# Performance work log

Measured on AMD Instinct MI355X. Metric: run time of the kernel, lower is better.

The kernel has to match this reference:

```python
import jax, jax.numpy as jnp
import numpy as np

B, S, H = 2, 2048, 2048
HK, HV, DK, DV, K = 16, 32, 128, 128, 4
KEY_DIM = HK * DK          # 2048
VAL_DIM = HV * DV          # 4096
CONV_DIM = 2 * KEY_DIM + VAL_DIM  # 8192
EPS = 1e-6


def setup_inputs() -> dict:
    key = jax.random.key(0)
    ks = jax.random.split(key, 8)
    n = lambda k, sh, s=1.0: jax.random.normal(k, sh, dtype=jnp.float32) * s
    return {
        "hidden_states": n(ks[0], (B, S, H)),
        "w_qkvz": n(ks[1], (H, 2 * KEY_DIM + 2 * VAL_DIM), 0.02),
        "w_ba": n(ks[2], (H, 2 * HV), 0.02),
        "conv_w": n(ks[3], (CONV_DIM, K), 0.5),
        "A_log": jnp.log(jax.random.uniform(ks[4], (HV,), minval=1e-3, maxval=16.0)),
        "dt_bias": jnp.ones((HV,), jnp.float32),
        "norm_w": jnp.ones((DV,), jnp.float32),
        "w_out": n(ks[5], (VAL_DIM, H), 0.02),
    }


def _l2norm(x):
    return x * jax.lax.rsqrt(jnp.sum(x * x, axis=-1, keepdims=True) + EPS)


def _softplus_thr(x, threshold=20.0):
    # fused_gdn_gating: softplus with linear tail beyond threshold (beta=1)
    return jnp.where(x <= threshold, jnp.log1p(jnp.exp(jnp.minimum(x, threshold))), x)


def reference(hidden_states, w_qkvz, w_ba, conv_w, A_log, dt_bias, norm_w, w_out):
    ratio = HV // HK  # v-heads per k-head (GVA)
    # --- projections + qkvz/ba split (fix_query_key_value_ordering) ---
    qkvz = (hidden_states @ w_qkvz).reshape(B, S, HK, 2 * DK + 2 * ratio * DV)
    q = qkvz[..., :DK]                                   # [B,S,HK,DK]
    k = qkvz[..., DK:2 * DK]
    v = qkvz[..., 2 * DK:2 * DK + ratio * DV]
    z = qkvz[..., 2 * DK + ratio * DV:].reshape(B, S, HV, DV)
    ba = (hidden_states @ w_ba).reshape(B, S, HK, 2 * ratio)
    b = ba[..., :ratio].reshape(B, S, HV)
    a = ba[..., ratio:].reshape(B, S, HV)
    # --- causal depthwise conv1d over time on cat(q,k,v), then SiLU ---
    mixed = jnp.concatenate([q.reshape(B, S, KEY_DIM), k.reshape(B, S, KEY_DIM),
                             v.reshape(B, S, VAL_DIM)], axis=-1)  # [B,S,CONV_DIM]
    xp = jnp.pad(mixed, ((0, 0), (K - 1, 0), (0, 0)))
    conv = sum(xp[:, j:j + S, :] * conv_w[:, j] for j in range(K))
    conv = jax.nn.silu(conv)
    q = _l2norm(conv[..., :KEY_DIM].reshape(B, S, HK, DK))
    k = _l2norm(conv[..., KEY_DIM:2 * KEY_DIM].reshape(B, S, HK, DK))
    v = conv[..., 2 * KEY_DIM:].reshape(B, S, HV, DV)
    q = jnp.repeat(q, ratio, axis=2)  # [B,S,HV,DK]
    k = jnp.repeat(k, ratio, axis=2)
    # --- gating: g = -exp(A_log) * softplus(a + dt_bias); beta = sigmoid(b) ---
    g = -jnp.exp(A_log) * _softplus_thr(a + dt_bias)   # [B,S,HV]
    beta = jax.nn.sigmoid(b)                            # [B,S,HV]
    scale = DK ** -0.5

    # --- gated delta rule recurrence over time ---
    def step(Sst, inp):
        qt, kt, vt, gt, bt = inp            # [B,HV,*]
        Sst = Sst * jnp.exp(gt)[..., None, None]
        kv = jnp.einsum('bhk,bhkv->bhv', kt, Sst)
        Sst = Sst + jnp.einsum('bhk,bhv->bhkv', kt, bt[..., None] * (vt - kv))
        o = jnp.einsum('bhk,bhkv->bhv', qt * scale, Sst)
        return Sst, o

    xs = (q.transpose(1, 0, 2, 3), k.transpose(1, 0, 2, 3), v.transpose(1, 0, 2, 3),
          g.transpose(1, 0, 2), beta.transpose(1, 0, 2))
    S0 = jnp.zeros((B, HV, DK, DV), jnp.float32)
    _, o = jax.lax.scan(step, S0, xs)
    core = o.transpose(1, 0, 2, 3)  # [B,S,HV,DV]
    # --- gated RMSNorm (norm before gate): rmsnorm(x)*w * silu(z) ---
    core_n = core * jax.lax.rsqrt(jnp.mean(core * core, axis=-1, keepdims=True) + EPS)
    y = core_n * norm_w * jax.nn.silu(z)
    # --- out projection ---
    return y.reshape(B, S, VAL_DIM) @ w_out
```

## Files before the change

### kernel.cpp

```cpp
#include <hip/hip_runtime.h>

typedef unsigned short u16;
typedef unsigned int u32;

typedef __attribute__((ext_vector_type(8))) short bf16x8;
typedef __attribute__((ext_vector_type(4))) float f32x4;
typedef __attribute__((ext_vector_type(2))) float f32x2;

__device__ __forceinline__ float bf2f(u16 v) {
    union { u32 i; float f; } u; u.i = ((u32)v) << 16; return u.f;
}
__device__ __forceinline__ u16 f2bf(float f) {
    union { float f; u32 i; } u; u.f = f;
    u32 r = u.i + 0x7FFFu + ((u.i >> 16) & 1u);
    return (u16)(r >> 16);
}
__device__ __forceinline__ u32 pack2(float lo, float hi) {
    return (u32)f2bf(lo) | ((u32)f2bf(hi) << 16);
}
__device__ __forceinline__ void unpack8(uint4 r, float* o) {
    o[0] = __uint_as_float(r.x << 16); o[1] = __uint_as_float(r.x & 0xffff0000u);
    o[2] = __uint_as_float(r.y << 16); o[3] = __uint_as_float(r.y & 0xffff0000u);
    o[4] = __uint_as_float(r.z << 16); o[5] = __uint_as_float(r.z & 0xffff0000u);
    o[6] = __uint_as_float(r.w << 16); o[7] = __uint_as_float(r.w & 0xffff0000u);
}
__device__ __forceinline__ void async16(const void* g, void* l) {
    __builtin_amdgcn_global_load_lds((const __attribute__((address_space(1))) void*)g,
                                     (__attribute__((address_space(3))) void*)l, 16, 0, 0);
}
template<int CTRL>
__device__ __forceinline__ float dpp_add(float x) {
    int y = __builtin_amdgcn_update_dpp(0, __float_as_int(x), CTRL, 0xf, 0xf, true);
    return x + __int_as_float(y);
}
__device__ __forceinline__ float row16_allreduce(float x) {
    x = dpp_add<0xB1>(x);
    x = dpp_add<0x4E>(x);
    x = dpp_add<0x141>(x);
    x = dpp_add<0x140>(x);
    return x;
}

__global__ __launch_bounds__(256) void f2b_kernel(const float* __restrict__ in,
                                                  u16* __restrict__ out)
{
    long i = ((long)blockIdx.x * 256 + threadIdx.x) * 8;
    float4 a = *(const float4*)&in[i], b = *(const float4*)&in[i + 4];
    uint4 o = make_uint4(pack2(a.x, a.y), pack2(a.z, a.w), pack2(b.x, b.y), pack2(b.z, b.w));
    *(uint4*)&out[i] = o;
}

__global__ __launch_bounds__(256) void transpose_f2b(const float* __restrict__ in,
                                                     u16* __restrict__ out, int R, int C)
{
    __shared__ float tile[32][33];
    const int r0 = blockIdx.y * 32, c0 = blockIdx.x * 32;
    const int tr = threadIdx.x >> 3;
    const int tc = (threadIdx.x & 7) * 4;
    float4 v = *(const float4*)&in[(long)(r0 + tr) * C + c0 + tc];
    tile[tr][tc] = v.x; tile[tr][tc + 1] = v.y; tile[tr][tc + 2] = v.z; tile[tr][tc + 3] = v.w;
    __syncthreads();
    uint2 o;
    o.x = pack2(tile[tc][tr], tile[tc + 1][tr]);
    o.y = pack2(tile[tc + 2][tr], tile[tc + 3][tr]);
    *(uint2*)&out[(long)(c0 + tr) * R + r0 + tc] = o;
}

template<int CF>
__global__ __launch_bounds__(256) void gemm_bt(const u16* __restrict__ A,
                                               const u16* __restrict__ Bt,
                                               void* __restrict__ Cp,
                                               void* __restrict__ Cp2,
                                               int M, int N, int K)
{
    __shared__ __align__(16) u16 As[128 * 32];
    __shared__ __align__(16) u16 Bs[128 * 32];

    const int tid = threadIdx.x;
    const int lane = tid & 63;
    const int wave = tid >> 6;
    const int wm = (wave >> 1) * 64;
    const int wn = (wave & 1) * 64;
    const int lanelo = lane & 15;
    const int quad = lane >> 4;
    const long m0 = (long)blockIdx.y * 128;
    const long n0 = (long)blockIdx.x * 128;

    f32x4 acc[4][4];
#pragma unroll
    for (int i = 0; i < 4; ++i)
#pragma unroll
        for (int j = 0; j < 4; ++j) acc[i][j] = (f32x4)0.0f;

    const u16* agp0 = A + (long)(m0 + wave * 16 + (lane >> 2)) * K + (lane & 3) * 8;
    const u16* agp1 = agp0 + 64 * (long)K;
    const u16* bgp0 = Bt + (long)(n0 + wave * 16 + (lane >> 2)) * K + (lane & 3) * 8;
    const u16* bgp1 = bgp0 + 64 * (long)K;
    u16* lA0 = &As[wave * 16 * 32];
    u16* lA1 = &As[(wave * 16 + 64) * 32];
    u16* lB0 = &Bs[wave * 16 * 32];
    u16* lB1 = &Bs[(wave * 16 + 64) * 32];

    for (int k0 = 0; k0 < K; k0 += 32) {
        __syncthreads();
        async16(agp0 + k0, lA0);
        async16(agp1 + k0, lA1);
        async16(bgp0 + k0, lB0);
        async16(bgp1 + k0, lB1);
        __syncthreads();

        bf16x8 af[4], bf[4];
#pragma unroll
        for (int mt = 0; mt < 4; ++mt)
            af[mt] = *(const bf16x8*)&As[(wm + mt * 16 + lanelo) * 32 + quad * 8];
#pragma unroll
        for (int nt = 0; nt < 4; ++nt)
            bf[nt] = *(const bf16x8*)&Bs[(wn + nt * 16 + lanelo) * 32 + quad * 8];
#pragma unroll
        for (int mt = 0; mt < 4; ++mt)
#pragma unroll
            for (int nt = 0; nt < 4; ++nt)
                acc[mt][nt] = __builtin_amdgcn_mfma_f32_16x16x32_bf16(af[mt], bf[nt], acc[mt][nt], 0, 0, 0);
    }

#pragma unroll
    for (int nt = 0; nt < 4; ++nt) {
        const long col = n0 + wn + nt * 16 + lanelo;
        int hkq = 0, rr = 0;
        if constexpr (CF == 2) { hkq = (int)col / 768; rr = (int)col - hkq * 768; }
#pragma unroll
        for (int mt = 0; mt < 4; ++mt)
#pragma unroll
            for (int r = 0; r < 4; ++r) {
                long row = m0 + wm + mt * 16 + quad * 4 + r;
                if constexpr (CF == 1)      ((float*)Cp)[row * N + col] = acc[mt][nt][r];
                else if constexpr (CF == 0) ((u16*)Cp)[row * N + col] = f2bf(acc[mt][nt][r]);
                else {
                    u16 vv = f2bf(acc[mt][nt][r]);
                    if (rr < 512) ((u16*)Cp )[row * 8192 + hkq * 512 + rr] = vv;
                    else          ((u16*)Cp2)[row * 4096 + hkq * 256 + (rr - 512)] = vv;
                }
            }
    }
}

__global__ __launch_bounds__(256) void ba_kernel(const float* __restrict__ hs,
                                                 const float* __restrict__ wba,
                                                 const float* __restrict__ A_log,
                                                 const float* __restrict__ dt_bias,
                                                 float* __restrict__ gbuf,
                                                 float* __restrict__ bbuf)
{
    const int m = blockIdx.x * 4 + (threadIdx.x >> 6);
    const int n = threadIdx.x & 63;
    const float* hrow = &hs[(long)m * 2048];
    float acc = 0.f;
#pragma unroll 8
    for (int k = 0; k < 2048; ++k)
        acc += hrow[k] * wba[(long)k * 64 + n];
    const int hk4 = n >> 2, r = n & 3;
    if (r < 2) {
        bbuf[(long)m * 32 + hk4 * 2 + r] = 1.f / (1.f + expf(-acc));
    } else {
        const int hv = hk4 * 2 + (r - 2);
        float x = acc + dt_bias[hv];
        float sp = (x > 20.f) ? x : log1pf(expf(x));
        gbuf[(long)m * 32 + hv] = -expf(A_log[hv]) * sp;
    }
}

__global__ __launch_bounds__(256) void conv_kernel(const u16* __restrict__ qkvb,
                                                   const float* __restrict__ cw,
                                                   u16* __restrict__ qfb,
                                                   u16* __restrict__ kfb,
                                                   u16* __restrict__ vbuf)
{
    const int bid = blockIdx.x;
    const int bs = bid >> 2, part = bid & 3;
    const int c = part * 2048 + threadIdx.x * 8;
    int n;
    if (c < 2048)       n = (c >> 7) * 512 + (c & 127);
    else if (c < 4096) { int c2 = c - 2048; n = (c2 >> 7) * 512 + 128 + (c2 & 127); }
    else               { int c2 = c - 4096; n = (c2 >> 8) * 512 + 256 + (c2 & 255); }
    const int s = bs & 2047;
    const long base = (long)bs * 8192 + n;

    float x0[8], x1[8], x2[8], x3[8];
#pragma unroll
    for (int i = 0; i < 8; ++i) { x0[i] = 0.f; x1[i] = 0.f; x2[i] = 0.f; }
    { uint4 r = *(const uint4*)&qkvb[base]; unpack8(r, x3); }
    if (s >= 1) { uint4 r = *(const uint4*)&qkvb[base - 8192];     unpack8(r, x2); }
    if (s >= 2) { uint4 r = *(const uint4*)&qkvb[base - 2 * 8192]; unpack8(r, x1); }
    if (s >= 3) { uint4 r = *(const uint4*)&qkvb[base - 3 * 8192]; unpack8(r, x0); }

    float v[8]; float ss = 0.f;
#pragma unroll
    for (int i = 0; i < 8; ++i) {
        float4 w = *(const float4*)&cw[(c + i) * 4];
        float a = x0[i] * w.x + x1[i] * w.y + x2[i] * w.z + x3[i] * w.w;
        v[i] = a / (1.f + expf(-a));
        ss += v[i] * v[i];
    }
    if (part < 2) {
        ss = row16_allreduce(ss);
        float rn = rsqrtf(ss + 1e-6f);
#pragma unroll
        for (int i = 0; i < 8; ++i) v[i] *= rn;
        u16* dst = (part == 0 ? qfb : kfb) + (long)bs * 2048 + (c & 2047);
        uint4 o = make_uint4(pack2(v[0], v[1]), pack2(v[2], v[3]), pack2(v[4], v[5]), pack2(v[6], v[7]));
        *(uint4*)dst = o;
    } else {
        uint4 o = make_uint4(pack2(v[0], v[1]), pack2(v[2], v[3]), pack2(v[4], v[5]), pack2(v[6], v[7]));
        *(uint4*)&vbuf[(long)bs * 4096 + (c - 4096)] = o;
    }
}


#define KL_S 136
#define KT_S 40
#define TL_S 40
#define GL_S 40
#define RT_S 40
#define SBT_S 136
#define SF_S 132
#define SCALE_QK 0.08838834764831845f

__global__ __launch_bounds__(64) void prep_kernel(const u16* __restrict__ kfb,
                                                  const float* __restrict__ gbuf,
                                                  const float* __restrict__ bbuf,
                                                  u16* __restrict__ Tbuf,
                                                  float* __restrict__ Cbuf)
{
    __shared__ __align__(16) u16 Kl[32 * KL_S];
    __shared__ __align__(16) float Lf[32 * 33];
    __shared__ __align__(16) float Tt[32 * 32];
    __shared__ float garr[32], barr[32], Gc[32];

    const int bid = blockIdx.x;
    const int b = bid >> 11, h = (bid >> 6) & 31, tile = bid & 63;
    const int hk = h >> 1;
    const int tid = threadIdx.x;
    const int lanelo = tid & 15, quad = tid >> 4;
    const long rowbase = (long)b * 2048 + tile * 32;

    {
        const int row = tid >> 1, half = tid & 1;
        const u16* src = &kfb[(rowbase + row) * 2048 + hk * 128 + half * 64];
#pragma unroll
        for (int i = 0; i < 8; ++i) {
            uint4 v = *(const uint4*)(src + i * 8);
            *(uint4*)&Kl[row * KL_S + half * 64 + i * 8] = v;
        }
    }
    if (tid < 32) {
        garr[tid] = gbuf[(rowbase + tid) * 32 + h];
        barr[tid] = bbuf[(rowbase + tid) * 32 + h];
    }
    __syncthreads();
    if (tid == 0) {
        float a = 0.f;
        for (int t = 0; t < 32; ++t) { a += garr[t]; Gc[t] = a; }
    }
    __syncthreads();

    f32x4 cc[2][2];
#pragma unroll
    for (int mt = 0; mt < 2; ++mt)
#pragma unroll
        for (int nt = 0; nt < 2; ++nt) cc[mt][nt] = (f32x4)0.f;
#pragma unroll
    for (int kt = 0; kt < 4; ++kt) {
        bf16x8 a0 = *(const bf16x8*)&Kl[(0 * 16 + lanelo) * KL_S + kt * 32 + quad * 8];
        bf16x8 a1 = *(const bf16x8*)&Kl[(1 * 16 + lanelo) * KL_S + kt * 32 + quad * 8];
        cc[0][0] = __builtin_amdgcn_mfma_f32_16x16x32_bf16(a0, a0, cc[0][0], 0, 0, 0);
        cc[0][1] = __builtin_amdgcn_mfma_f32_16x16x32_bf16(a0, a1, cc[0][1], 0, 0, 0);
        cc[1][0] = __builtin_amdgcn_mfma_f32_16x16x32_bf16(a1, a0, cc[1][0], 0, 0, 0);
        cc[1][1] = __builtin_amdgcn_mfma_f32_16x16x32_bf16(a1, a1, cc[1][1], 0, 0, 0);
    }
#pragma unroll
    for (int mt = 0; mt < 2; ++mt)
#pragma unroll
        for (int nt = 0; nt < 2; ++nt)
#pragma unroll
            for (int r = 0; r < 4; ++r) {
                const int t = mt * 16 + quad * 4 + r, j = nt * 16 + lanelo;
                float L = (j < t) ? barr[t] * __expf(Gc[t] - Gc[j]) * cc[mt][nt][r] : 0.f;
                Lf[t * 33 + j] = L;
            }
    __syncthreads();

    if (tid < 32) {
        const int c = tid;
        float T[32];
#pragma unroll
        for (int t = 0; t < 32; ++t) {
            float s = (t == c) ? 1.f : 0.f;
#pragma unroll
            for (int j = 0; j < t; ++j) s -= Lf[t * 33 + j] * T[j];
            T[t] = s;
        }
#pragma unroll
        for (int t = 0; t < 32; ++t) Tt[t * 32 + c] = T[t];
    }
    if (tid < 32) {
        const float G31 = Gc[31];
        const float eg = __expf(Gc[tid]);
        float* cb = &Cbuf[(long)bid * 256];
        cb[tid]       = barr[tid];
        cb[32 + tid]  = barr[tid] * eg;
        cb[64 + tid]  = SCALE_QK * eg;
        cb[96 + tid]  = __expf(G31 - Gc[tid]);
        cb[128 + tid] = Gc[tid];
        if (tid == 0) cb[192] = __expf(G31);
    }
    __syncthreads();
    {
        const float* tp = &Tt[tid * 16];
        u32 hi[8], lo[8];
#pragma unroll
        for (int i = 0; i < 8; ++i) {
            u16 h0 = f2bf(tp[2 * i]),     h1 = f2bf(tp[2 * i + 1]);
            float l0 = tp[2 * i] - bf2f(h0), l1 = tp[2 * i + 1] - bf2f(h1);
            hi[i] = (u32)h0 | ((u32)h1 << 16);
            lo[i] = pack2(l0, l1);
        }
        u16* dst = &Tbuf[(long)bid * 2048 + tid * 16];
        *(uint4*)dst       = make_uint4(hi[0], hi[1], hi[2], hi[3]);
        *(uint4*)(dst + 8) = make_uint4(hi[4], hi[5], hi[6], hi[7]);
        u16* dstl = dst + 1024;
        *(uint4*)dstl       = make_uint4(lo[0], lo[1], lo[2], lo[3]);
        *(uint4*)(dstl + 8) = make_uint4(lo[4], lo[5], lo[6], lo[7]);
    }
}

__global__ __launch_bounds__(256) void scan_kernel(const u16* __restrict__ kfb,
                                                   const u16* __restrict__ qfb,
                                                   const u16* __restrict__ vbuf,
                                                   const u16* __restrict__ Tbuf,
                                                   const float* __restrict__ Cbuf,
                                                   u16* __restrict__ obuf)
{
    __shared__ __align__(16) u16 Kl[32 * KL_S];
    __shared__ __align__(16) u16 Ql[32 * KL_S];
    __shared__ __align__(16) u16 KTl[128 * KT_S];
    __shared__ __align__(16) u16 Tl[64 * TL_S];
    __shared__ __align__(16) u16 Gl[32 * GL_S];
    __shared__ __align__(16) u16 RTl[16 * RT_S];
    __shared__ __align__(16) u16 DTl[16 * RT_S];
    __shared__ __align__(16) u16 DTs[16 * RT_S];
    __shared__ __align__(16) u16 Sbt[16 * SBT_S];
    __shared__ __align__(16) float Sf[16 * SF_S];
    __shared__ __align__(16) u16 Vl[32 * 16];
    __shared__ __align__(16) float Cf[256];

    const int bid = blockIdx.x;
    const int b = bid >> 8;
    const int h = (bid >> 3) & 31;
    const int c0 = (bid & 7) * 16;
    const int hk = h >> 1;
    const int tid = threadIdx.x;
    const int lane = tid & 63;
    const int w = tid >> 6;
    const int lanelo = lane & 15;
    const int quad = lane >> 4;
    const long rowbase = (long)b * 2048;
    const long tIdxBase = ((long)(b * 32 + h)) * 64;

    for (int i = tid; i < 16 * SF_S; i += 256) Sf[i] = 0.f;
    for (int i = tid; i < 16 * SBT_S; i += 256) Sbt[i] = 0;
    __syncthreads();

    const int srow = tid >> 3, scp = tid & 7;
    const u16* kg = &kfb[(rowbase + srow) * 2048 + hk * 128 + scp * 16];
    const u16* qg = &qfb[(rowbase + srow) * 2048 + hk * 128 + scp * 16];
    const int mtQK = w >> 1, ntQK = w & 1;
    const int mtY = w & 1;
    const bool isY = (w < 2);

    for (int tile = 0; tile < 64; ++tile) {
        const int t0 = tile * 32;
        uint4 k0 = *(const uint4*)(kg + (long)t0 * 2048);
        uint4 k1 = *(const uint4*)(kg + (long)t0 * 2048 + 8);
        uint4 q0 = *(const uint4*)(qg + (long)t0 * 2048);
        uint4 q1 = *(const uint4*)(qg + (long)t0 * 2048 + 8);
        uint4 tt = *(const uint4*)&Tbuf[(tIdxBase + tile) * 2048 + tid * 8];
        if (w == 0) {
            const int r = tid >> 1, c8 = (tid & 1) * 8;
            async16(&vbuf[(rowbase + t0 + r) * 4096 + h * 128 + c0 + c8], &Vl[tid * 8]);
        } else if (w == 1) {
            const int u = tid - 64;
            async16(&Cbuf[(tIdxBase + tile) * 256 + u * 4], &Cf[u * 4]);
        }
        *(uint4*)&Kl[srow * KL_S + scp * 16] = k0;
        *(uint4*)&Kl[srow * KL_S + scp * 16 + 8] = k1;
        *(uint4*)&Ql[srow * KL_S + scp * 16] = q0;
        *(uint4*)&Ql[srow * KL_S + scp * 16 + 8] = q1;
        {
            u32 ws_[8] = { k0.x, k0.y, k0.z, k0.w, k1.x, k1.y, k1.z, k1.w };
#pragma unroll
            for (int i = 0; i < 8; ++i) {
                KTl[(scp * 16 + 2 * i) * KT_S + srow] = (u16)(ws_[i] & 0xffffu);
                KTl[(scp * 16 + 2 * i + 1) * KT_S + srow] = (u16)(ws_[i] >> 16);
            }
        }
        {
            const int r = tid >> 2, c8 = (tid & 3) * 8;
            *(uint4*)&Tl[r * TL_S + c8] = tt;
        }
        __syncthreads();

        f32x4 qk = (f32x4)0.f;
#pragma unroll
        for (int kt = 0; kt < 4; ++kt) {
            bf16x8 aq = *(const bf16x8*)&Ql[(mtQK * 16 + lanelo) * KL_S + kt * 32 + quad * 8];
            bf16x8 bk = *(const bf16x8*)&Kl[(ntQK * 16 + lanelo) * KL_S + kt * 32 + quad * 8];
            qk = __builtin_amdgcn_mfma_f32_16x16x32_bf16(aq, bk, qk, 0, 0, 0);
        }
        const u16* aYsrc = isY ? Kl : Ql;
        f32x4 yo = (f32x4)0.f;
#pragma unroll
        for (int kt = 0; kt < 4; ++kt) {
            bf16x8 a = *(const bf16x8*)&aYsrc[(mtY * 16 + lanelo) * KL_S + kt * 32 + quad * 8];
            bf16x8 bs = *(const bf16x8*)&Sbt[lanelo * SBT_S + kt * 32 + quad * 8];
            yo = __builtin_amdgcn_mfma_f32_16x16x32_bf16(a, bs, yo, 0, 0, 0);
        }
        {
            f32x4 gt4 = *(const f32x4*)&Cf[128 + mtQK * 16 + quad * 4];
            float gj = Cf[128 + ntQK * 16 + lanelo];
#pragma unroll
            for (int r = 0; r < 4; ++r) {
                const int t = mtQK * 16 + quad * 4 + r, j = ntQK * 16 + lanelo;
                float gv = (j <= t) ? qk[r] * __expf(gt4[r] - gj) * SCALE_QK : 0.f;
                Gl[t * GL_S + j] = f2bf(gv);
            }
        }
        if (isY) {
            f32x4 bt4 = *(const f32x4*)&Cf[0 + mtY * 16 + quad * 4];
            f32x4 bg4 = *(const f32x4*)&Cf[32 + mtY * 16 + quad * 4];
            float rv[4];
#pragma unroll
            for (int r = 0; r < 4; ++r) {
                float vv = bf2f(Vl[(mtY * 16 + quad * 4 + r) * 16 + lanelo]);
                rv[r] = bt4[r] * vv - bg4[r] * yo[r];
            }
            *(uint2*)&RTl[lanelo * RT_S + mtY * 16 + quad * 4] =
                make_uint2(pack2(rv[0], rv[1]), pack2(rv[2], rv[3]));
        }
        __syncthreads();

        if (isY) {
            bf16x8 ath = *(const bf16x8*)&Tl[(mtY * 16 + lanelo) * TL_S + quad * 8];
            bf16x8 atl = *(const bf16x8*)&Tl[(32 + mtY * 16 + lanelo) * TL_S + quad * 8];
            bf16x8 br  = *(const bf16x8*)&RTl[lanelo * RT_S + quad * 8];
            f32x4 dl = __builtin_amdgcn_mfma_f32_16x16x32_bf16(ath, br, (f32x4)0.f, 0, 0, 0);
            dl = __builtin_amdgcn_mfma_f32_16x16x32_bf16(atl, br, dl, 0, 0, 0);
            f32x4 ec4 = *(const f32x4*)&Cf[96 + mtY * 16 + quad * 4];
            *(uint2*)&DTl[lanelo * RT_S + mtY * 16 + quad * 4] =
                make_uint2(pack2(dl[0], dl[1]), pack2(dl[2], dl[3]));
            *(uint2*)&DTs[lanelo * RT_S + mtY * 16 + quad * 4] =
                make_uint2(pack2(dl[0] * ec4[0], dl[1] * ec4[1]),
                           pack2(dl[2] * ec4[2], dl[3] * ec4[3]));
        }
        __syncthreads();

        if (!isY) {
            const int mt = w - 2;
            bf16x8 ag = *(const bf16x8*)&Gl[(mt * 16 + lanelo) * GL_S + quad * 8];
            bf16x8 bd = *(const bf16x8*)&DTl[lanelo * RT_S + quad * 8];
            f32x4 oi = __builtin_amdgcn_mfma_f32_16x16x32_bf16(ag, bd, (f32x4)0.f, 0, 0, 0);
            f32x4 so4 = *(const f32x4*)&Cf[64 + mt * 16 + quad * 4];
#pragma unroll
            for (int r = 0; r < 4; ++r) {
                float ov = so4[r] * yo[r] + oi[r];
                obuf[((rowbase + t0 + mt * 16 + quad * 4 + r) * 32 + h) * 128 + c0 + lanelo] = f2bf(ov);
            }
        }
        const float gC = Cf[192];
#pragma unroll
        for (int s = 0; s < 2; ++s) {
            const int mt = w * 2 + s;
            bf16x8 ak = *(const bf16x8*)&KTl[(mt * 16 + lanelo) * KT_S + quad * 8];
            bf16x8 bd = *(const bf16x8*)&DTs[lanelo * RT_S + quad * 8];
            f32x4 ds4 = __builtin_amdgcn_mfma_f32_16x16x32_bf16(ak, bd, (f32x4)0.f, 0, 0, 0);
            float* sp = &Sf[lanelo * SF_S + mt * 16 + quad * 4];
            f32x4 sv = *(const f32x4*)sp;
#pragma unroll
            for (int r = 0; r < 4; ++r) sv[r] = gC * sv[r] + ds4[r];
            *(f32x4*)sp = sv;
            *(uint2*)&Sbt[lanelo * SBT_S + mt * 16 + quad * 4] =
                make_uint2(pack2(sv[0], sv[1]), pack2(sv[2], sv[3]));
        }
        __syncthreads();
    }
}

__global__ __launch_bounds__(128) void gate_kernel(const u16* __restrict__ obuf,
                                                   const u16* __restrict__ zbuf,
                                                   const float* __restrict__ norm_w,
                                                   u16* __restrict__ ybuf)
{
    const int bid = blockIdx.x;
    const int bs = bid >> 5, hv = bid & 31;
    const int dv = threadIdx.x;
    __shared__ float red[2];
    float v = bf2f(obuf[(long)bid * 128 + dv]);
    float ss = v * v;
    ss += __shfl_xor(ss, 1);  ss += __shfl_xor(ss, 2);  ss += __shfl_xor(ss, 4);
    ss += __shfl_xor(ss, 8);  ss += __shfl_xor(ss, 16); ss += __shfl_xor(ss, 32);
    if ((dv & 63) == 0) red[dv >> 6] = ss;
    __syncthreads();
    const float mean = (red[0] + red[1]) * (1.f / 128.f);
    const float rstd = rsqrtf(mean + 1e-6f);
    const int hk = hv >> 1;
    const float z = bf2f(zbuf[(long)bs * 4096 + hk * 256 + (hv & 1) * 128 + dv]);
    const float y = v * rstd * norm_w[dv] * (z / (1.f + expf(-z)));
    ybuf[(long)bs * 4096 + hv * 128 + dv] = f2bf(y);
}

extern "C" void kernel_launch(void* const* d_in, const int* in_sizes, int n_in,
                              void* d_out, int out_size, void* d_ws, size_t ws_size,
                              hipStream_t stream)
{
    const float* hs      = (const float*)d_in[0];
    const float* w_qkvz  = (const float*)d_in[1];
    const float* w_ba    = (const float*)d_in[2];
    const float* conv_w  = (const float*)d_in[3];
    const float* A_log   = (const float*)d_in[4];
    const float* dt_bias = (const float*)d_in[5];
    const float* norm_w  = (const float*)d_in[6];
    const float* w_out   = (const float*)d_in[7];

    char* ws = (char*)d_ws;
    u16*   qkvb  = (u16*)ws;
    u16*   kfb   = (u16*)(ws + 67108864);
    u16*   qfb   = (u16*)(ws + 83886080);
    u16*   vbuf  = (u16*)(ws + 100663296);
    u16*   Tbuf  = (u16*)(ws + 134217728);
    float* Cbuf  = (float*)(ws + 150994944);
    float* gbuf  = (float*)(ws + 155189248);
    float* bbuf  = (float*)(ws + 155713536);
    u16*   zbuf  = (u16*)(ws + 156237824);
    u16*   wqkvz_t = (u16*)(ws + 67108864);
    u16*   hs_b    = (u16*)(ws + 117440512);
    u16*   obuf    = (u16*)ws;
    u16*   wout_t  = (u16*)(ws + 33554432);
    u16*   ybuf    = (u16*)(ws + 67108864);

    f2b_kernel<<<4096, 256, 0, stream>>>(hs, hs_b);
    transpose_f2b<<<dim3(384, 64), 256, 0, stream>>>(w_qkvz, wqkvz_t, 2048, 12288);
    gemm_bt<2><<<dim3(96, 32), 256, 0, stream>>>(hs_b, wqkvz_t, qkvb, zbuf, 4096, 12288, 2048);
    ba_kernel<<<1024, 256, 0, stream>>>(hs, w_ba, A_log, dt_bias, gbuf, bbuf);
    conv_kernel<<<4096 * 4, 256, 0, stream>>>(qkvb, conv_w, qfb, kfb, vbuf);
    prep_kernel<<<4096, 64, 0, stream>>>(kfb, gbuf, bbuf, Tbuf, Cbuf);
    scan_kernel<<<512, 256, 0, stream>>>(kfb, qfb, vbuf, Tbuf, Cbuf, obuf);
    transpose_f2b<<<dim3(64, 128), 256, 0, stream>>>(w_out, wout_t, 4096, 2048);
    gate_kernel<<<4096 * 32, 128, 0, stream>>>(obuf, zbuf, norm_w, ybuf);
    gemm_bt<1><<<dim3(16, 32), 256, 0, stream>>>(ybuf, wout_t, d_out, nullptr, 4096, 2048, 4096);
}
```

Baseline: 1.033 ms.

## Add 256x256 double-buffered swizzled GEMM for the qkvz projection

Replaces the 128x128-tile GEMM for the large qkvz projection with a new kernel that uses 256x256 tiles, 512 threads, and double-buffered async LDS loads with an XOR-swizzled layout. It also adds workgroup-order swizzling for L2 locality and raises MFMA priority with s_setprio. The goal is more data reuse per tile and fewer LDS bank conflicts. In exchange it needs 128KB of LDS and heavy register use, which limits occupancy, and it launches only 768 workgroups.

```diff
diff --git a/kernel.cpp b/kernel.cpp
--- a/kernel.cpp
+++ b/kernel.cpp
@@ -126,20 +126,114 @@
 #pragma unroll
     for (int nt = 0; nt < 4; ++nt) {
         const long col = n0 + wn + nt * 16 + lanelo;
-        int hkq = 0, rr = 0;
-        if constexpr (CF == 2) { hkq = (int)col / 768; rr = (int)col - hkq * 768; }
 #pragma unroll
         for (int mt = 0; mt < 4; ++mt)
 #pragma unroll
             for (int r = 0; r < 4; ++r) {
                 long row = m0 + wm + mt * 16 + quad * 4 + r;
                 if constexpr (CF == 1)      ((float*)Cp)[row * N + col] = acc[mt][nt][r];
-                else if constexpr (CF == 0) ((u16*)Cp)[row * N + col] = f2bf(acc[mt][nt][r]);
-                else {
-                    u16 vv = f2bf(acc[mt][nt][r]);
-                    if (rr < 512) ((u16*)Cp )[row * 8192 + hkq * 512 + rr] = vv;
-                    else          ((u16*)Cp2)[row * 4096 + hkq * 256 + (rr - 512)] = vv;
-                }
+                else                        ((u16*)Cp)[row * N + col] = f2bf(acc[mt][nt][r]);
+            }
+    }
+}
+
+__global__ __launch_bounds__(512, 2) void gemm256_bt(const u16* __restrict__ A,
+                                                     const u16* __restrict__ Bt,
+                                                     void* __restrict__ Cp,
+                                                     void* __restrict__ Cp2,
+                                                     int M, int N, int K)
+{
+    __shared__ __align__(16) u16 As[2][256 * 64];
+    __shared__ __align__(16) u16 Bs[2][256 * 64];
+
+    const int tid = threadIdx.x;
+    const int lane = tid & 63;
+    const int w = tid >> 6;
+    const int wm = w >> 2;
+    const int wn = w & 3;
+    const int lanelo = lane & 15;
+    const int quad = lane >> 4;
+
+    const int nx = gridDim.x;
+    const int nwg = nx * gridDim.y;
+    const int orig = blockIdx.y * nx + blockIdx.x;
+    const int cpx = nwg >> 3;
+    const int swz = (orig & 7) * cpx + (orig >> 3);
+    const long n0 = (long)(swz % nx) * 256;
+    const long m0 = (long)(swz / nx) * 256;
+
+    f32x4 acc[8][4];
+#pragma unroll
+    for (int i = 0; i < 8; ++i)
+#pragma unroll
+        for (int j = 0; j < 4; ++j) acc[i][j] = (f32x4)0.0f;
+
+    const int kt_n = K >> 6;
+
+    auto stage = [&](int buf, int kt) {
+        const int k0 = kt << 6;
+#pragma unroll
+        for (int r = 0; r < 4; ++r) {
+            const int c = r * 512 + tid;
+            const int row = c >> 3, ci = c & 7;
+            const int gcol = ((ci ^ (row & 7)) << 3);
+            async16(&A[(m0 + row) * (long)K + k0 + gcol], &As[buf][c * 8]);
+        }
+#pragma unroll
+        for (int r = 0; r < 4; ++r) {
+            const int c = r * 512 + tid;
+            const int row = c >> 3, ci = c & 7;
+            const int gcol = ((ci ^ (row & 7)) << 3);
+            async16(&Bt[(n0 + row) * (long)K + k0 + gcol], &Bs[buf][c * 8]);
+        }
+    };
+
+    int buf = 0;
+    stage(0, 0);
+    __syncthreads();
+
+    for (int kt = 0; kt < kt_n; ++kt) {
+        if (kt + 1 < kt_n) stage(buf ^ 1, kt + 1);
+#pragma unroll
+        for (int kk = 0; kk < 2; ++kk) {
+            bf16x8 a[8], b[4];
+#pragma unroll
+            for (int mf = 0; mf < 8; ++mf) {
+                const int row = wm * 128 + mf * 16 + lanelo;
+                const int ci = (kk * 4 + quad) ^ (row & 7);
+                a[mf] = *(const bf16x8*)&As[buf][row * 64 + ci * 8];
+            }
+#pragma unroll
+            for (int nf = 0; nf < 4; ++nf) {
+                const int row = wn * 64 + nf * 16 + lanelo;
+                const int ci = (kk * 4 + quad) ^ (row & 7);
+                b[nf] = *(const bf16x8*)&Bs[buf][row * 64 + ci * 8];
+            }
+            __builtin_amdgcn_s_setprio(1);
+#pragma unroll
+            for (int mf = 0; mf < 8; ++mf)
+#pragma unroll
+                for (int nf = 0; nf < 4; ++nf)
+                    acc[mf][nf] = __builtin_amdgcn_mfma_f32_16x16x32_bf16(a[mf], b[nf], acc[mf][nf], 0, 0, 0);
+            __builtin_amdgcn_s_setprio(0);
+        }
+        __syncthreads();
+        buf ^= 1;
+    }
+
+#pragma unroll
+    for (int nf = 0; nf < 4; ++nf) {
+        const long col = n0 + wn * 64 + nf * 16 + lanelo;
+        const int hkq = (int)col / 768;
+        const int rr = (int)col - hkq * 768;
+#pragma unroll
+        for (int mf = 0; mf < 8; ++mf)
+#pragma unroll
+            for (int r = 0; r < 4; ++r) {
+                const long row = m0 + wm * 128 + mf * 16 + quad * 4 + r;
+                const u16 vv = f2bf(acc[mf][nf][r]);
+                if (rr < 512) ((u16*)Cp )[row * 8192 + hkq * 512 + rr] = vv;
+                else          ((u16*)Cp2)[row * 4096 + hkq * 256 + (rr - 512)] = vv;
             }
     }
 }
@@ -548,7 +642,7 @@
 
     f2b_kernel<<<4096, 256, 0, stream>>>(hs, hs_b);
     transpose_f2b<<<dim3(384, 64), 256, 0, stream>>>(w_qkvz, wqkvz_t, 2048, 12288);
-    gemm_bt<2><<<dim3(96, 32), 256, 0, stream>>>(hs_b, wqkvz_t, qkvb, zbuf, 4096, 12288, 2048);
+    gemm256_bt<<<dim3(48, 16), 512, 0, stream>>>(hs_b, wqkvz_t, qkvb, zbuf, 4096, 12288, 2048);
     ba_kernel<<<1024, 256, 0, stream>>>(hs, w_ba, A_log, dt_bias, gbuf, bbuf);
     conv_kernel<<<4096 * 4, 256, 0, stream>>>(qkvb, conv_w, qfb, kfb, vbuf);
     prep_kernel<<<4096, 64, 0, stream>>>(kfb, gbuf, bbuf, Tbuf, Cbuf);
```

Result: faster. 1.010 ms (-2.2%).
